# Kernel tuning notes

Hardware: AMD Instinct MI355X
Metric: run time of the kernel (lower is better)

## Reference

```python
import jax, jax.numpy as jnp
import numpy as np

B, L, D = 64, 4096, 1024
FILL = -10000.0  # sentinel used by the original masked_fill before the sort


def setup_inputs() -> dict:
    key = jax.random.key(0)
    k1, k2 = jax.random.split(key)
    features = jax.random.normal(k1, (B, L, D), dtype=jnp.float32)
    lengths = jax.random.randint(k2, (B,), 0, L, dtype=jnp.int32)
    return {"features": features, "lengths": lengths}


def reference(features, lengths):
    # Original: mask invalid positions with -10000, sort descending along seq,
    # zero out masked slots, take element 0. Mathematically this is a masked
    # max over valid positions (and 0 if a sequence has length 0, since the
    # second masked_fill zeroes position 0 when mask[:,0] is False).
    L_ = features.shape[1]
    mask = jnp.arange(L_)[None, :] < lengths[:, None]            # [B, L]
    masked = jnp.where(mask[:, :, None], features, FILL)          # [B, L, D]
    pooled = jnp.max(masked, axis=1)                              # [B, D]
    pooled = jnp.where((lengths > 0)[:, None], pooled, 0.0)
    pool_weights = None
    return pooled
```

## Files before the change

kernel.cpp:

```cpp
#include <hip/hip_runtime.h>

#define FILLV (-10000.0f)

typedef __attribute__((ext_vector_type(4))) float f32x4;

__device__ __forceinline__ f32x4 vmax4(f32x4 a, f32x4 b) {
    f32x4 r;
    r.x = fmaxf(a.x, b.x);
    r.y = fmaxf(a.y, b.y);
    r.z = fmaxf(a.z, b.z);
    r.w = fmaxf(a.w, b.w);
    return r;
}

__device__ __forceinline__ f32x4 ntload(const f32x4* p) {
    return __builtin_nontemporal_load(p);
}

__device__ __forceinline__ f32x4 fillv4() {
    f32x4 v = {FILLV, FILLV, FILLV, FILLV};
    return v;
}


__global__ __launch_bounds__(256, 4)
void feasel_rows_partial_kernel(const float* __restrict__ feat,
                                const int* __restrict__ lengths,
                                float* __restrict__ part,
                                int B, int L, int DV, int G) {
    __shared__ int rowstart[1025];
    __shared__ int slotbase[1025];
    const int t = threadIdx.x;
    const int j = blockIdx.x;

    if (t == 0) {
        rowstart[0] = 0;
        for (int b = 0; b < B; ++b) {
            int len = lengths[b];
            len = len < 0 ? 0 : (len > L ? L : len);
            rowstart[b + 1] = rowstart[b] + len;
        }
    }
    __syncthreads();
    const int W = rowstart[B];

    for (int b = t; b < B; b += blockDim.x) {
        int s = 0;
        if (W > 0 && rowstart[b + 1] > rowstart[b]) {
            int jlo = (int)((unsigned long long)rowstart[b] * G / W);
            int jhi = (int)((unsigned long long)(rowstart[b + 1] - 1) * G / W);
            s = jhi - jlo + 1;
        }
        slotbase[b + 1] = s;
    }
    __syncthreads();
    if (t == 0) {
        slotbase[0] = 0;
        for (int b = 0; b < B; ++b) slotbase[b + 1] += slotbase[b];
    }
    __syncthreads();

    if (W == 0) return;
    const int r0 = (int)(((unsigned long long)W * j + G - 1) / G);
    int       r1 = (int)(((unsigned long long)W * (j + 1) + G - 1) / G);
    if (r1 > W) r1 = W;
    if (r0 >= r1) return;

    int lo = 0, hi = B;
    while (hi - lo > 1) {
        int m = (lo + hi) >> 1;
        if (rowstart[m] <= r0) lo = m; else hi = m;
    }
    int b = lo;
    int r = r0;

    while (r < r1) {
        while (rowstart[b + 1] <= r) ++b;
        const int rend  = min(r1, rowstart[b + 1]);
        const int nrows = rend - r;
        const int l     = r - rowstart[b];

        const f32x4* __restrict__ p =
            reinterpret_cast<const f32x4*>(feat) + ((size_t)b * L + l) * DV + t;

        f32x4 a0 = fillv4(), a1 = fillv4(), a2 = fillv4(), a3 = fillv4();
        f32x4 a4 = fillv4(), a5 = fillv4(), a6 = fillv4(), a7 = fillv4();

        int k = 0;
        for (; k + 16 <= nrows; k += 16) {
            f32x4 v0  = ntload(p +  0 * (size_t)DV);
            f32x4 v1  = ntload(p +  1 * (size_t)DV);
            f32x4 v2  = ntload(p +  2 * (size_t)DV);
            f32x4 v3  = ntload(p +  3 * (size_t)DV);
            f32x4 v4  = ntload(p +  4 * (size_t)DV);
            f32x4 v5  = ntload(p +  5 * (size_t)DV);
            f32x4 v6  = ntload(p +  6 * (size_t)DV);
            f32x4 v7  = ntload(p +  7 * (size_t)DV);
            f32x4 v8  = ntload(p +  8 * (size_t)DV);
            f32x4 v9  = ntload(p +  9 * (size_t)DV);
            f32x4 v10 = ntload(p + 10 * (size_t)DV);
            f32x4 v11 = ntload(p + 11 * (size_t)DV);
            f32x4 v12 = ntload(p + 12 * (size_t)DV);
            f32x4 v13 = ntload(p + 13 * (size_t)DV);
            f32x4 v14 = ntload(p + 14 * (size_t)DV);
            f32x4 v15 = ntload(p + 15 * (size_t)DV);
            a0 = vmax4(a0, vmax4(v0,  v8));
            a1 = vmax4(a1, vmax4(v1,  v9));
            a2 = vmax4(a2, vmax4(v2,  v10));
            a3 = vmax4(a3, vmax4(v3,  v11));
            a4 = vmax4(a4, vmax4(v4,  v12));
            a5 = vmax4(a5, vmax4(v5,  v13));
            a6 = vmax4(a6, vmax4(v6,  v14));
            a7 = vmax4(a7, vmax4(v7,  v15));
            p += 16 * (size_t)DV;
        }
        for (; k + 4 <= nrows; k += 4) {
            a0 = vmax4(a0, ntload(p + 0 * (size_t)DV));
            a1 = vmax4(a1, ntload(p + 1 * (size_t)DV));
            a2 = vmax4(a2, ntload(p + 2 * (size_t)DV));
            a3 = vmax4(a3, ntload(p + 3 * (size_t)DV));
            p += 4 * (size_t)DV;
        }
        for (; k < nrows; ++k) {
            a0 = vmax4(a0, ntload(p));
            p += DV;
        }
        a0 = vmax4(a0, a1);
        a2 = vmax4(a2, a3);
        a4 = vmax4(a4, a5);
        a6 = vmax4(a6, a7);
        a0 = vmax4(vmax4(a0, a2), vmax4(a4, a6));

        const int jlo  = (int)((unsigned long long)rowstart[b] * G / W);
        const int slot = slotbase[b] + (j - jlo);
        reinterpret_cast<f32x4*>(part)[(size_t)slot * DV + t] = a0;

        r = rend;
    }
}

__global__ void feasel_rows_reduce_kernel(const float* __restrict__ part,
                                          const int* __restrict__ lengths,
                                          float* __restrict__ out,
                                          int B, int L, int DV, int G) {
    __shared__ int rowstart[1025];
    __shared__ int slotbase[1025];
    const int t = threadIdx.x;

    if (t == 0) {
        rowstart[0] = 0;
        for (int bb = 0; bb < B; ++bb) {
            int len = lengths[bb];
            len = len < 0 ? 0 : (len > L ? L : len);
            rowstart[bb + 1] = rowstart[bb] + len;
        }
    }
    __syncthreads();
    const int W = rowstart[B];
    for (int bb = t; bb < B; bb += blockDim.x) {
        int s = 0;
        if (W > 0 && rowstart[bb + 1] > rowstart[bb]) {
            int jlo = (int)((unsigned long long)rowstart[bb] * G / W);
            int jhi = (int)((unsigned long long)(rowstart[bb + 1] - 1) * G / W);
            s = jhi - jlo + 1;
        }
        slotbase[bb + 1] = s;
    }
    __syncthreads();
    if (t == 0) {
        slotbase[0] = 0;
        for (int bb = 0; bb < B; ++bb) slotbase[bb + 1] += slotbase[bb];
    }
    __syncthreads();

    const int b = blockIdx.x;
    const int c = blockIdx.y * 64 + t;
    if (c >= DV) return;

    const int rb0 = rowstart[b], rb1 = rowstart[b + 1];
    f32x4 acc;
    if (rb1 <= rb0) {
        f32x4 z = {0.f, 0.f, 0.f, 0.f};
        acc = z;
    } else {
        const int jlo = (int)((unsigned long long)rb0 * G / W);
        const int jhi = (int)((unsigned long long)(rb1 - 1) * G / W);
        acc = fillv4();
        for (int j = jlo; j <= jhi; ++j) {
            int br0 = (int)(((unsigned long long)W * j + G - 1) / G);
            int br1 = (int)(((unsigned long long)W * (j + 1) + G - 1) / G);
            if (br1 > W) br1 = W;
            const int is = br0 > rb0 ? br0 : rb0;
            const int ie = br1 < rb1 ? br1 : rb1;
            if (is < ie) {
                const int slot = slotbase[b] + (j - jlo);
                acc = vmax4(acc,
                    reinterpret_cast<const f32x4*>(part)[(size_t)slot * DV + c]);
            }
        }
    }
    reinterpret_cast<f32x4*>(out)[(size_t)b * DV + c] = acc;
}

__global__ void feasel_direct_kernel(const float* __restrict__ feat,
                                     const int* __restrict__ lengths,
                                     float* __restrict__ out,
                                     int L, int DV) {
    const int b = blockIdx.x;
    const int t = threadIdx.x;
    int len = lengths[b];
    len = len < 0 ? 0 : (len > L ? L : len);

    const f32x4* __restrict__ p =
        reinterpret_cast<const f32x4*>(feat) + (size_t)b * L * DV + t;

    f32x4 a0 = fillv4(), a1 = fillv4(), a2 = fillv4(), a3 = fillv4();
    int l = 0;
    for (; l + 4 <= len; l += 4) {
        a0 = vmax4(a0, ntload(p + 0 * (size_t)DV));
        a1 = vmax4(a1, ntload(p + 1 * (size_t)DV));
        a2 = vmax4(a2, ntload(p + 2 * (size_t)DV));
        a3 = vmax4(a3, ntload(p + 3 * (size_t)DV));
        p += 4 * (size_t)DV;
    }
    for (; l < len; ++l) {
        a0 = vmax4(a0, ntload(p));
        p += DV;
    }
    a0 = vmax4(vmax4(a0, a1), vmax4(a2, a3));
    if (len <= 0) {
        f32x4 z = {0.f, 0.f, 0.f, 0.f};
        a0 = z;
    }
    reinterpret_cast<f32x4*>(out)[(size_t)b * DV + t] = a0;
}

extern "C" void kernel_launch(void* const* d_in, const int* in_sizes, int n_in,
                              void* d_out, int out_size, void* d_ws, size_t ws_size,
                              hipStream_t stream) {
    const float* feat    = (const float*)d_in[0];
    const int*   lengths = (const int*)d_in[1];
    float*       out     = (float*)d_out;

    const int B  = in_sizes[1];
    const int D  = out_size / B;
    const int DV = D / 4;
    const int L  = in_sizes[0] / (B * D);
    const int G  = 1024;

    const size_t part_bytes = (size_t)(G + B) * D * sizeof(float);

    if (part_bytes <= ws_size && B <= 1024) {
        float* part = (float*)d_ws;

        feasel_rows_partial_kernel<<<G, 256, 0, stream>>>(feat, lengths, part,
                                                          B, L, DV, G);

        dim3 grid2(B, (DV + 63) / 64);
        feasel_rows_reduce_kernel<<<grid2, 64, 0, stream>>>(part, lengths, out,
                                                            B, L, DV, G);
    } else {
        feasel_direct_kernel<<<B, DV, 0, stream>>>(feat, lengths, out, L, DV);
    }
}
```

Measured before the change: 100.1 us.

## Fuse partial and reduce kernels using atomic last-block reduction per row

Merges the two-kernel split-reduction into a single launch. Each block writes its partial max, then bumps a per-sequence atomic counter, and the last block to finish reduces that sequence's partials into the output. Extra blocks zero the outputs of empty sequences, and a memset clears the counters beforehand. This removes the second launch and the reduce kernel's redundant prefix recomputation, at the cost of a memset launch, threadfences and extra per-segment syncs inside the main kernel.

```diff
diff --git a/kernel.cpp b/kernel.cpp
--- a/kernel.cpp
+++ b/kernel.cpp
@@ -22,16 +22,28 @@
     return v;
 }
 
-
 __global__ __launch_bounds__(256, 4)
-void feasel_rows_partial_kernel(const float* __restrict__ feat,
-                                const int* __restrict__ lengths,
-                                float* __restrict__ part,
-                                int B, int L, int DV, int G) {
+void feasel_fused_kernel(const float* __restrict__ feat,
+                         const int* __restrict__ lengths,
+                         float* __restrict__ part,
+                         int* __restrict__ counters,
+                         float* __restrict__ out,
+                         int B, int L, int DV, int G) {
+    const int t  = threadIdx.x;
+    const int j  = blockIdx.x;
+
+    if (j >= G) {
+        const int b = j - G;
+        if (lengths[b] <= 0) {
+            f32x4 z = {0.f, 0.f, 0.f, 0.f};
+            reinterpret_cast<f32x4*>(out)[(size_t)b * DV + t] = z;
+        }
+        return;
+    }
+
     __shared__ int rowstart[1025];
     __shared__ int slotbase[1025];
-    const int t = threadIdx.x;
-    const int j = blockIdx.x;
+    __shared__ int isLastSh;
 
     if (t == 0) {
         rowstart[0] = 0;
@@ -43,12 +55,15 @@
     }
     __syncthreads();
     const int W = rowstart[B];
+    if (W == 0) return;
+    const int Ge = W < G ? W : G;
+    if (j >= Ge) return;
 
     for (int b = t; b < B; b += blockDim.x) {
         int s = 0;
-        if (W > 0 && rowstart[b + 1] > rowstart[b]) {
-            int jlo = (int)((unsigned long long)rowstart[b] * G / W);
-            int jhi = (int)((unsigned long long)(rowstart[b + 1] - 1) * G / W);
+        if (rowstart[b + 1] > rowstart[b]) {
+            int jlo = (int)((unsigned long long)rowstart[b] * Ge / W);
+            int jhi = (int)((unsigned long long)(rowstart[b + 1] - 1) * Ge / W);
             s = jhi - jlo + 1;
         }
         slotbase[b + 1] = s;
@@ -60,9 +75,8 @@
     }
     __syncthreads();
 
-    if (W == 0) return;
-    const int r0 = (int)(((unsigned long long)W * j + G - 1) / G);
-    int       r1 = (int)(((unsigned long long)W * (j + 1) + G - 1) / G);
+    const int r0 = (int)(((unsigned long long)W * j + Ge - 1) / Ge);
+    int       r1 = (int)(((unsigned long long)W * (j + 1) + Ge - 1) / Ge);
     if (r1 > W) r1 = W;
     if (r0 >= r1) return;
 
@@ -131,75 +145,30 @@
         a6 = vmax4(a6, a7);
         a0 = vmax4(vmax4(a0, a2), vmax4(a4, a6));
 
-        const int jlo  = (int)((unsigned long long)rowstart[b] * G / W);
-        const int slot = slotbase[b] + (j - jlo);
-        reinterpret_cast<f32x4*>(part)[(size_t)slot * DV + t] = a0;
+        const int jlo = (int)((unsigned long long)rowstart[b] * Ge / W);
+        const int jhi = (int)((unsigned long long)(rowstart[b + 1] - 1) * Ge / W);
+        const int sb  = slotbase[b];
+
+        reinterpret_cast<f32x4*>(part)[(size_t)(sb + (j - jlo)) * DV + t] = a0;
+        __threadfence();
+        if (t == 0) {
+            const int target = jhi - jlo + 1;
+            const int old    = atomicAdd(&counters[b], 1);
+            isLastSh = (old == target - 1) ? 1 : 0;
+        }
+        __syncthreads();
+        if (isLastSh) {
+            __threadfence();
+            f32x4 acc = fillv4();
+            for (int jj = jlo; jj <= jhi; ++jj)
+                acc = vmax4(acc,
+                    reinterpret_cast<const f32x4*>(part)[(size_t)(sb + (jj - jlo)) * DV + t]);
+            reinterpret_cast<f32x4*>(out)[(size_t)b * DV + t] = acc;
+        }
+        __syncthreads();
 
         r = rend;
     }
-}
-
-__global__ void feasel_rows_reduce_kernel(const float* __restrict__ part,
-                                          const int* __restrict__ lengths,
-                                          float* __restrict__ out,
-                                          int B, int L, int DV, int G) {
-    __shared__ int rowstart[1025];
-    __shared__ int slotbase[1025];
-    const int t = threadIdx.x;
-
-    if (t == 0) {
-        rowstart[0] = 0;
-        for (int bb = 0; bb < B; ++bb) {
-            int len = lengths[bb];
-            len = len < 0 ? 0 : (len > L ? L : len);
-            rowstart[bb + 1] = rowstart[bb] + len;
-        }
-    }
-    __syncthreads();
-    const int W = rowstart[B];
-    for (int bb = t; bb < B; bb += blockDim.x) {
-        int s = 0;
-        if (W > 0 && rowstart[bb + 1] > rowstart[bb]) {
-            int jlo = (int)((unsigned long long)rowstart[bb] * G / W);
-            int jhi = (int)((unsigned long long)(rowstart[bb + 1] - 1) * G / W);
-            s = jhi - jlo + 1;
-        }
-        slotbase[bb + 1] = s;
-    }
-    __syncthreads();
-    if (t == 0) {
-        slotbase[0] = 0;
-        for (int bb = 0; bb < B; ++bb) slotbase[bb + 1] += slotbase[bb];
-    }
-    __syncthreads();
-
-    const int b = blockIdx.x;
-    const int c = blockIdx.y * 64 + t;
-    if (c >= DV) return;
-
-    const int rb0 = rowstart[b], rb1 = rowstart[b + 1];
-    f32x4 acc;
-    if (rb1 <= rb0) {
-        f32x4 z = {0.f, 0.f, 0.f, 0.f};
-        acc = z;
-    } else {
-        const int jlo = (int)((unsigned long long)rb0 * G / W);
-        const int jhi = (int)((unsigned long long)(rb1 - 1) * G / W);
-        acc = fillv4();
-        for (int j = jlo; j <= jhi; ++j) {
-            int br0 = (int)(((unsigned long long)W * j + G - 1) / G);
-            int br1 = (int)(((unsigned long long)W * (j + 1) + G - 1) / G);
-            if (br1 > W) br1 = W;
-            const int is = br0 > rb0 ? br0 : rb0;
-            const int ie = br1 < rb1 ? br1 : rb1;
-            if (is < ie) {
-                const int slot = slotbase[b] + (j - jlo);
-                acc = vmax4(acc,
-                    reinterpret_cast<const f32x4*>(part)[(size_t)slot * DV + c]);
-            }
-        }
-    }
-    reinterpret_cast<f32x4*>(out)[(size_t)b * DV + c] = acc;
 }
 
 __global__ void feasel_direct_kernel(const float* __restrict__ feat,
@@ -249,16 +218,17 @@
     const int G  = 1024;
 
     const size_t part_bytes = (size_t)(G + B) * D * sizeof(float);
-
-    if (part_bytes <= ws_size && B <= 1024) {
-        float* part = (float*)d_ws;
-
-        feasel_rows_partial_kernel<<<G, 256, 0, stream>>>(feat, lengths, part,
-                                                          B, L, DV, G);
-
-        dim3 grid2(B, (DV + 63) / 64);
-        feasel_rows_reduce_kernel<<<grid2, 64, 0, stream>>>(part, lengths, out,
-                                                            B, L, DV, G);
+    const size_t need       = part_bytes + (size_t)B * sizeof(int);
+
+    if (need <= ws_size && B <= 1024 && DV <= 256) {
+        float* part     = (float*)d_ws;
+        int*   counters = (int*)((char*)d_ws + part_bytes);
+
+        hipMemsetAsync(counters, 0, (size_t)B * sizeof(int), stream);
+
+        feasel_fused_kernel<<<G + B, DV, 0, stream>>>(feat, lengths, part,
+                                                      counters, out,
+                                                      B, L, DV, G);
     } else {
         feasel_direct_kernel<<<B, DV, 0, stream>>>(feat, lengths, out, L, DV);
     }
```

Result: slower. 263.9 us (+163.7%).
